# Kernel optimization log

Hardware: AMD Instinct MI355X
Metric: run time of the kernel (lower is better)

The kernel has to match this reference:

```python
import jax, jax.numpy as jnp
import numpy as np
from jax import lax


def setup_inputs() -> dict:
    key = jax.random.key(0)
    k1, k2 = jax.random.split(key)
    x = jax.random.normal(k1, (32, 128, 64, 64), dtype=jnp.float32)
    # learned kernel, original shape (k, k, in_channels, out_channels)
    K = jax.random.normal(k2, (3, 3, 128, 256), dtype=jnp.float32) * 0.05
    return {"x": x, "K": K}


def reference(x, K):
    stride, padding = 1, 1
    kh = K.shape[0]
    C = K.shape[2]
    O = K.shape[3]
    H = x.shape[-1]
    P = H + 2 * padding
    out_size = (P - kh) // stride + 1
    # Original pairs x-patches flattened as (C, kh, kw) with K flattened
    # row-major as (kh, kw, C), matched purely by flat index. Equivalent to a
    # standard conv with the weight buffer reinterpreted as (C, kh, kw, O):
    W = K.reshape(-1, O).reshape(C, kh, kh, O).transpose(3, 0, 1, 2)  # (O,C,kh,kw)
    out = lax.conv_general_dilated(
        x, W,
        window_strides=(stride, stride),
        padding=[(padding, padding), (padding, padding)],
        dimension_numbers=("NCHW", "OIHW", "NCHW"),
    )  # (B, O, out_size, out_size)
    # Original loop uses range(0, P - kh, stride) (missing +1): when
    # (P - kh) % stride == 0 the last output row/col is never written (stays 0).
    n_filled = -(-(P - kh) // stride)  # ceil((P-kh)/stride), static
    if n_filled < out_size:
        out = out.at[:, :, n_filled:, :].set(0.0)
        out = out.at[:, :, :, n_filled:].set(0.0)
    return out
```

## Files before the change

### kernel.cpp

```cpp
#include <hip/hip_runtime.h>
#include <hip/hip_bf16.h>

typedef __attribute__((ext_vector_type(8))) short bf16x8;
typedef __attribute__((ext_vector_type(4))) float f32x4;

#define CIN   128
#define HW    64
#define OUTC  256

#define BP_OFF     33554432ULL
#define ZP_OFF     34144256ULL
#define WS_NEEDED  34148352ULL

#define SB  __builtin_amdgcn_s_barrier()
#define SCB __builtin_amdgcn_sched_barrier(0)
#define WAITV(N) asm volatile("s_waitcnt vmcnt(" #N ")" ::: "memory")
#define MFMA(a, b, c) __builtin_amdgcn_mfma_f32_16x16x32_bf16(a, b, c, 0, 0, 0)

__global__ __launch_bounds__(256) void conv_prep(const float* __restrict__ X,
                                                 const float* __restrict__ Kw,
                                                 __hip_bfloat16* __restrict__ Xt2,
                                                 __hip_bfloat16* __restrict__ Bp2,
                                                 __hip_bfloat16* __restrict__ zp) {
    const int blk = blockIdx.x;
    if (blk < 2048) {
        __shared__ __hip_bfloat16 L[64][136];
        const int b = blk >> 6;
        const int y = blk & 63;
        const int x = threadIdx.x & 63;
        const int c0 = (threadIdx.x >> 6) * 32;
        const float* src = X + (((long)(b * CIN + c0) * HW + y) * HW + x);
        #pragma unroll
        for (int j = 0; j < 32; j += 2) {
            float v0 = src[(long)j * (HW * HW)];
            float v1 = src[(long)(j + 1) * (HW * HW)];
            __hip_bfloat162 p;
            p.x = __float2bfloat16(v0);
            p.y = __float2bfloat16(v1);
            *reinterpret_cast<__hip_bfloat162*>(&L[x][c0 + j]) = p;
        }
        __syncthreads();
        const int xx = threadIdx.x >> 2;
        const int g  = threadIdx.x & 3;
        #pragma unroll
        for (int cc = 0; cc < 4; ++cc) {
            bf16x8 v = *reinterpret_cast<const bf16x8*>(&L[xx][cc * 32 + g * 8]);
            long dst = (((long)(b * 4 + cc) * 64 + y) * 64 + xx) * 32 + g * 8;
            *reinterpret_cast<bf16x8*>(&Xt2[dst]) = v;
        }
    } else if (blk < 2112) {
        for (int i = (blk - 2048) * 256 + threadIdx.x; i < 294912; i += 64 * 256) {
            int c32 = i & 31;
            int n   = (i >> 5) & 255;
            int cc  = (i >> 13) & 3;
            int ij  = i >> 15;
            int c   = cc * 32 + c32;
            Bp2[i] = __float2bfloat16(Kw[(c * 9 + ij) * 256 + n]);
        }
    } else {
        *reinterpret_cast<float4*>((char*)zp + threadIdx.x * 16) = float4{0.f, 0.f, 0.f, 0.f};
    }
}

__global__ __launch_bounds__(256, 2) void conv_igemm8(
    const __hip_bfloat16* __restrict__ Xt2,
    const __hip_bfloat16* __restrict__ Bp2,
    const __hip_bfloat16* __restrict__ zp,
    float* __restrict__ out)
{
    __shared__ __hip_bfloat16 As[3][128 * 32];
    __shared__ __hip_bfloat16 Bs[3][256 * 32];

    const int tid  = threadIdx.x;
    const int wv   = tid >> 6;
    const int lane = tid & 63;
    const int l16  = lane & 15;
    const int d16  = lane >> 4;

    const int bid   = blockIdx.x;
    const int mtile = (bid & 7) * 128 + (bid >> 3);
    const int b  = mtile >> 5;
    const int y0 = (mtile & 31) * 2;

    const int srow = lane >> 2;
    const int sg   = lane & 3;

    f32x4 acc[8][4] = {};

    const int G = (sg - (srow >> 1)) & 3;

    const int rA0 = wv * 32 + srow;
    const int rA1 = rA0 + 16;
    const int xA0 = rA0 & 63, xA1 = rA1 & 63;
    const int yA0 = y0 + (rA0 >> 6), yA1 = y0 + (rA1 >> 6);
    const __hip_bfloat16* pA0 = Xt2 + (((long)b * 16384 + yA0 * 64 + xA0) * 32 + G * 8);
    const __hip_bfloat16* pA1 = Xt2 + (((long)b * 16384 + yA1 * 64 + xA1) * 32 + G * 8);
    const __hip_bfloat16* zpg = zp + G * 8;
    const int rB0 = wv * 64 + srow;
    const __hip_bfloat16* pB = Bp2 + ((long)rB0 * 32 + G * 8);
    const int ldsA0 = (wv * 32) * 32;
    const int ldsA1 = (wv * 32 + 16) * 32;
    const int ldsB0 = (wv * 64) * 32;

    auto stage = [&](int S) {
        const int ij = S >> 2;
        const int cc = S & 3;
        const int di = ij / 3 - 1;
        const int dj = ij % 3 - 1;
        const int rs = S % 3;
        const long offA = ((long)cc * 4096 + di * 64 + dj) * 32;
        const bool ok0 = ((unsigned)(xA0 + dj) < 64u) && ((unsigned)(yA0 + di) < 64u);
        const bool ok1 = ((unsigned)(xA1 + dj) < 64u) && ((unsigned)(yA1 + di) < 64u);
        const __hip_bfloat16* gA0 = ok0 ? pA0 + offA : zpg;
        const __hip_bfloat16* gA1 = ok1 ? pA1 + offA : zpg;
        __hip_bfloat16* ldsA = &As[rs][0];
        __builtin_amdgcn_global_load_lds(
            (const __attribute__((address_space(1))) void*)gA0,
            (__attribute__((address_space(3))) void*)(ldsA + ldsA0), 16, 0, 0);
        __builtin_amdgcn_global_load_lds(
            (const __attribute__((address_space(1))) void*)gA1,
            (__attribute__((address_space(3))) void*)(ldsA + ldsA1), 16, 0, 0);
        const long offB = (long)(ij * 4 + cc) * 8192;
        __hip_bfloat16* ldsB = &Bs[rs][0];
        #pragma unroll
        for (int l = 0; l < 4; ++l) {
            __builtin_amdgcn_global_load_lds(
                (const __attribute__((address_space(1))) void*)(pB + offB + l * 512),
                (__attribute__((address_space(3))) void*)(ldsB + ldsB0 + l * 512), 16, 0, 0);
        }
    };

    stage(0); stage(1);
    WAITV(6);
    SCB; SB;

    #pragma unroll
    for (int H = 0; H < 36; ++H) {
        const int RB = H % 3;
        bf16x8 Af[8], Bf[4];
        #pragma unroll
        for (int mi = 0; mi < 8; ++mi) {
            const int m = mi * 16 + l16;
            const int s = (d16 + (m >> 1)) & 3;
            Af[mi] = *reinterpret_cast<const bf16x8*>(&As[RB][m * 32 + s * 8]);
        }
        #pragma unroll
        for (int ni = 0; ni < 4; ++ni) {
            const int n = wv * 64 + ni * 16 + l16;
            const int s = (d16 + (n >> 1)) & 3;
            Bf[ni] = *reinterpret_cast<const bf16x8*>(&Bs[RB][n * 32 + s * 8]);
        }
        if (H < 34) stage(H + 2);
        if (H < 34)       WAITV(12);
        else if (H == 34) WAITV(6);
        else              WAITV(0);
        SCB; SB;
        __builtin_amdgcn_s_setprio(1);
        #pragma unroll
        for (int ni = 0; ni < 4; ++ni)
            #pragma unroll
            for (int mi = 0; mi < 8; ++mi)
                acc[mi][ni] = MFMA(Af[mi], Bf[ni], acc[mi][ni]);
        __builtin_amdgcn_s_setprio(0);
        SCB; SB;
    }

    #pragma unroll
    for (int mi = 0; mi < 8; ++mi) {
        const int m  = mi * 16 + d16 * 4;
        const int x0 = m & 63;
        const int y  = y0 + (m >> 6);
        #pragma unroll
        for (int ni = 0; ni < 4; ++ni) {
            const int o = wv * 64 + ni * 16 + l16;
            float4 v;
            v.x = acc[mi][ni][0];
            v.y = acc[mi][ni][1];
            v.z = acc[mi][ni][2];
            v.w = acc[mi][ni][3];
            if (y == HW - 1) { v.x = v.y = v.z = v.w = 0.f; }
            if (x0 + 3 == HW - 1) v.w = 0.f;
            *reinterpret_cast<float4*>(
                out + ((long)(b * OUTC + o) * 4096 + y * 64 + x0)) = v;
        }
    }
}

__global__ __launch_bounds__(256) void conv_igemm_bf16(
    const float* __restrict__ X, const float* __restrict__ Kw, float* __restrict__ out) {
    __shared__ __hip_bfloat16 As[128][40];
    __shared__ __hip_bfloat16 Bs[128][40];
    const int tid = threadIdx.x, wave = tid >> 6, lane = tid & 63;
    const int l16 = lane & 15, d16 = lane >> 4;
    const int m_base = blockIdx.x * 128;
    const int b = m_base >> 12, y0 = (m_base & 4095) >> 6;
    const int n_base = blockIdx.y * 128;
    const int wm = (wave >> 1) * 64, wn = (wave & 1) * 64;
    f32x4 acc[4][4] = {};
    const int smm = tid & 127, ccb = tid >> 7;
    const int sx = smm & 63, syr = smm >> 6;
    for (int ij = 0; ij < 9; ++ij) {
        const int di = ij / 3 - 1, dj = ij % 3 - 1;
        const int xp = sx + dj, yp = y0 + syr + di;
        const bool ok = ((unsigned)xp < 64u) && ((unsigned)yp < 64u);
        const long xbase = (((long)b * CIN) * HW + yp) * HW + xp;
        for (int c0 = 0; c0 < CIN; c0 += 32) {
            for (int cc = ccb; cc < 32; cc += 2) {
                float v = ok ? X[xbase + (long)(c0 + cc) * 4096] : 0.f;
                As[smm][cc] = __float2bfloat16(v);
                Bs[smm][cc] = __float2bfloat16(Kw[((c0 + cc) * 9 + ij) * OUTC + n_base + smm]);
            }
            __syncthreads();
            bf16x8 afrag[4], bfrag[4];
            for (int mi = 0; mi < 4; ++mi)
                afrag[mi] = *reinterpret_cast<const bf16x8*>(&As[wm + mi * 16 + l16][d16 * 8]);
            for (int ni = 0; ni < 4; ++ni)
                bfrag[ni] = *reinterpret_cast<const bf16x8*>(&Bs[wn + ni * 16 + l16][d16 * 8]);
            for (int mi = 0; mi < 4; ++mi)
                for (int ni = 0; ni < 4; ++ni)
                    acc[mi][ni] = __builtin_amdgcn_mfma_f32_16x16x32_bf16(
                        afrag[mi], bfrag[ni], acc[mi][ni], 0, 0, 0);
            __syncthreads();
        }
    }
    for (int mi = 0; mi < 4; ++mi)
        for (int ni = 0; ni < 4; ++ni)
            for (int r = 0; r < 4; ++r) {
                const int mm = wm + mi * 16 + d16 * 4 + r;
                const int nn = wn + ni * 16 + l16;
                const int y = y0 + (mm >> 6), x = mm & 63, o = n_base + nn;
                float v = acc[mi][ni][r];
                if (y == 63 || x == 63) v = 0.f;
                out[(((long)b * OUTC + o) * HW + y) * HW + x] = v;
            }
}

extern "C" void kernel_launch(void* const* d_in, const int* in_sizes, int n_in,
                              void* d_out, int out_size, void* d_ws, size_t ws_size,
                              hipStream_t stream) {
    const float* X  = (const float*)d_in[0];
    const float* Kw = (const float*)d_in[1];
    float* out = (float*)d_out;

    if (ws_size >= WS_NEEDED) {
        char* ws = (char*)d_ws;
        __hip_bfloat16* Xt2 = (__hip_bfloat16*)ws;
        __hip_bfloat16* Bp2 = (__hip_bfloat16*)(ws + BP_OFF);
        __hip_bfloat16* zp  = (__hip_bfloat16*)(ws + ZP_OFF);
        conv_prep<<<dim3(2113), dim3(256), 0, stream>>>(X, Kw, Xt2, Bp2, zp);
        conv_igemm8<<<dim3(1024), dim3(256), 0, stream>>>(Xt2, Bp2, zp, out);
    } else {
        conv_igemm_bf16<<<dim3(1024, 2), dim3(256), 0, stream>>>(X, Kw, out);
    }
}
```

Measured before the change: 106.8 us.

## Load MFMA operands directly from global memory into registers, dropping LDS staging

```diff
diff --git a/kernel.cpp b/kernel.cpp
--- a/kernel.cpp
+++ b/kernel.cpp
@@ -12,9 +12,6 @@
 #define ZP_OFF     34144256ULL
 #define WS_NEEDED  34148352ULL
 
-#define SB  __builtin_amdgcn_s_barrier()
-#define SCB __builtin_amdgcn_sched_barrier(0)
-#define WAITV(N) asm volatile("s_waitcnt vmcnt(" #N ")" ::: "memory")
 #define MFMA(a, b, c) __builtin_amdgcn_mfma_f32_16x16x32_bf16(a, b, c, 0, 0, 0)
 
 __global__ __launch_bounds__(256) void conv_prep(const float* __restrict__ X,
@@ -62,15 +59,12 @@
     }
 }
 
-__global__ __launch_bounds__(256, 2) void conv_igemm8(
+__global__ __launch_bounds__(256, 2) void conv_igemm9(
     const __hip_bfloat16* __restrict__ Xt2,
     const __hip_bfloat16* __restrict__ Bp2,
     const __hip_bfloat16* __restrict__ zp,
     float* __restrict__ out)
 {
-    __shared__ __hip_bfloat16 As[3][128 * 32];
-    __shared__ __hip_bfloat16 Bs[3][256 * 32];
-
     const int tid  = threadIdx.x;
     const int wv   = tid >> 6;
     const int lane = tid & 63;
@@ -82,87 +76,55 @@
     const int b  = mtile >> 5;
     const int y0 = (mtile & 31) * 2;
 
-    const int srow = lane >> 2;
-    const int sg   = lane & 3;
-
     f32x4 acc[8][4] = {};
 
-    const int G = (sg - (srow >> 1)) & 3;
-
-    const int rA0 = wv * 32 + srow;
-    const int rA1 = rA0 + 16;
-    const int xA0 = rA0 & 63, xA1 = rA1 & 63;
-    const int yA0 = y0 + (rA0 >> 6), yA1 = y0 + (rA1 >> 6);
-    const __hip_bfloat16* pA0 = Xt2 + (((long)b * 16384 + yA0 * 64 + xA0) * 32 + G * 8);
-    const __hip_bfloat16* pA1 = Xt2 + (((long)b * 16384 + yA1 * 64 + xA1) * 32 + G * 8);
-    const __hip_bfloat16* zpg = zp + G * 8;
-    const int rB0 = wv * 64 + srow;
-    const __hip_bfloat16* pB = Bp2 + ((long)rB0 * 32 + G * 8);
-    const int ldsA0 = (wv * 32) * 32;
-    const int ldsA1 = (wv * 32 + 16) * 32;
-    const int ldsB0 = (wv * 64) * 32;
-
-    auto stage = [&](int S) {
-        const int ij = S >> 2;
-        const int cc = S & 3;
-        const int di = ij / 3 - 1;
-        const int dj = ij % 3 - 1;
-        const int rs = S % 3;
-        const long offA = ((long)cc * 4096 + di * 64 + dj) * 32;
-        const bool ok0 = ((unsigned)(xA0 + dj) < 64u) && ((unsigned)(yA0 + di) < 64u);
-        const bool ok1 = ((unsigned)(xA1 + dj) < 64u) && ((unsigned)(yA1 + di) < 64u);
-        const __hip_bfloat16* gA0 = ok0 ? pA0 + offA : zpg;
-        const __hip_bfloat16* gA1 = ok1 ? pA1 + offA : zpg;
-        __hip_bfloat16* ldsA = &As[rs][0];
-        __builtin_amdgcn_global_load_lds(
-            (const __attribute__((address_space(1))) void*)gA0,
-            (__attribute__((address_space(3))) void*)(ldsA + ldsA0), 16, 0, 0);
-        __builtin_amdgcn_global_load_lds(
-            (const __attribute__((address_space(1))) void*)gA1,
-            (__attribute__((address_space(3))) void*)(ldsA + ldsA1), 16, 0, 0);
-        const long offB = (long)(ij * 4 + cc) * 8192;
-        __hip_bfloat16* ldsB = &Bs[rs][0];
-        #pragma unroll
-        for (int l = 0; l < 4; ++l) {
-            __builtin_amdgcn_global_load_lds(
-                (const __attribute__((address_space(1))) void*)(pB + offB + l * 512),
-                (__attribute__((address_space(3))) void*)(ldsB + ldsB0 + l * 512), 16, 0, 0);
-        }
+    const __hip_bfloat16* PA = Xt2 + (((long)b * 16384 + y0 * 64 + l16) * 32 + d16 * 8);
+    const __hip_bfloat16* PB = Bp2 + ((long)(wv * 64 + l16) * 32 + d16 * 8);
+    const __hip_bfloat16* PZ = zp + d16 * 8;
+
+    auto loadA = [&](int mi, int H) -> bf16x8 {
+        const int ij = H >> 2, cc = H & 3;
+        const int di = ij / 3 - 1, dj = ij % 3 - 1;
+        bool ok = true;
+        if (dj == 1)  ok = ((mi & 3) != 3) || (l16 != 15);
+        if (dj == -1) ok = ((mi & 3) != 0) || (l16 != 0);
+        if (di == 1)  ok = ok && (y0 + (mi >> 2) < 63);
+        if (di == -1) ok = ok && (y0 + (mi >> 2) > 0);
+        const long off = (long)(cc * 4096 + di * 64 + dj) * 32
+                       + (long)((mi & 3) * 16 + (mi >> 2) * 64) * 32;
+        const __hip_bfloat16* p = ok ? PA + off : PZ;
+        return *reinterpret_cast<const bf16x8*>(p);
     };
-
-    stage(0); stage(1);
-    WAITV(6);
-    SCB; SB;
+    auto loadB = [&](int ni, int H) -> bf16x8 {
+        const int ij = H >> 2, cc = H & 3;
+        const long off = (long)(ij * 4 + cc) * 8192 + ni * 512;
+        return *reinterpret_cast<const bf16x8*>(PB + off);
+    };
+
+    bf16x8 Af[8], Bf[2][4];
+
+    #pragma unroll
+    for (int mi = 0; mi < 8; ++mi) Af[mi] = loadA(mi, 0);
+    #pragma unroll
+    for (int ni = 0; ni < 4; ++ni) Bf[0][ni] = loadB(ni, 0);
 
     #pragma unroll
     for (int H = 0; H < 36; ++H) {
-        const int RB = H % 3;
-        bf16x8 Af[8], Bf[4];
+        const int cb = H & 1;
+        if (H < 35) {
+            #pragma unroll
+            for (int ni = 0; ni < 4; ++ni) Bf[cb ^ 1][ni] = loadB(ni, H + 1);
+        }
+        __builtin_amdgcn_s_setprio(1);
         #pragma unroll
         for (int mi = 0; mi < 8; ++mi) {
-            const int m = mi * 16 + l16;
-            const int s = (d16 + (m >> 1)) & 3;
-            Af[mi] = *reinterpret_cast<const bf16x8*>(&As[RB][m * 32 + s * 8]);
-        }
-        #pragma unroll
-        for (int ni = 0; ni < 4; ++ni) {
-            const int n = wv * 64 + ni * 16 + l16;
-            const int s = (d16 + (n >> 1)) & 3;
-            Bf[ni] = *reinterpret_cast<const bf16x8*>(&Bs[RB][n * 32 + s * 8]);
-        }
-        if (H < 34) stage(H + 2);
-        if (H < 34)       WAITV(12);
-        else if (H == 34) WAITV(6);
-        else              WAITV(0);
-        SCB; SB;
-        __builtin_amdgcn_s_setprio(1);
-        #pragma unroll
-        for (int ni = 0; ni < 4; ++ni)
-            #pragma unroll
-            for (int mi = 0; mi < 8; ++mi)
-                acc[mi][ni] = MFMA(Af[mi], Bf[ni], acc[mi][ni]);
+            acc[mi][0] = MFMA(Af[mi], Bf[cb][0], acc[mi][0]);
+            acc[mi][1] = MFMA(Af[mi], Bf[cb][1], acc[mi][1]);
+            acc[mi][2] = MFMA(Af[mi], Bf[cb][2], acc[mi][2]);
+            acc[mi][3] = MFMA(Af[mi], Bf[cb][3], acc[mi][3]);
+            if (H < 35) Af[mi] = loadA(mi, H + 1);
+        }
         __builtin_amdgcn_s_setprio(0);
-        SCB; SB;
     }
 
     #pragma unroll
@@ -248,7 +210,7 @@
         __hip_bfloat16* Bp2 = (__hip_bfloat16*)(ws + BP_OFF);
         __hip_bfloat16* zp  = (__hip_bfloat16*)(ws + ZP_OFF);
         conv_prep<<<dim3(2113), dim3(256), 0, stream>>>(X, Kw, Xt2, Bp2, zp);
-        conv_igemm8<<<dim3(1024), dim3(256), 0, stream>>>(Xt2, Bp2, zp, out);
+        conv_igemm9<<<dim3(1024), dim3(256), 0, stream>>>(Xt2, Bp2, zp, out);
     } else {
         conv_igemm_bf16<<<dim3(1024, 2), dim3(256), 0, stream>>>(X, Kw, out);
     }
```

New measurement: 136.5 us. +27.8%, slower.
